# Performance work log

Hardware: AMD Instinct MI355X
Metric: run time of the kernel (lower is better)

## Reference

```python
import jax, jax.numpy as jnp
import numpy as np
import math

N_WAY, K_SHOT, Q_QUERY, PRJ_NUM, D = 5, 5, 15, 6, 64


def setup_inputs() -> dict:
    key = jax.random.key(0)
    k1, k2 = jax.random.split(key)
    feat = jax.random.normal(k1, (600, 64, 10, 10), dtype=jnp.float32)
    label = jax.random.randint(k2, (450,), 0, N_WAY)
    scale = jnp.ones((1,), dtype=jnp.float32)
    r = jnp.zeros((2,), dtype=jnp.float32)
    return {"feat": feat, "label": label, "scale": scale, "r": r}


def reference(feat, label, scale, r):
    ns = N_WAY * K_SHOT * PRJ_NUM  # 150 support images
    inv_sqrt_d = 1.0 / math.sqrt(D)
    support_xf = feat[:ns] * inv_sqrt_d
    query_xf = feat[ns:] * inv_sqrt_d
    q, c, h, w = query_xf.shape

    # support: (n_way, k_shot*prj_num*h*w, c)
    support = support_xf.reshape(N_WAY, K_SHOT * PRJ_NUM, c, h * w)
    support = jnp.transpose(support, (0, 1, 3, 2)).reshape(N_WAY, -1, c)
    # query: (q*h*w, c)
    query = jnp.transpose(query_xf.reshape(q, c, h * w), (0, 2, 1)).reshape(q * h * w, c)

    alpha, beta = r[0], r[1]
    reg = support.shape[1] / support.shape[2]
    lam = reg * jnp.exp(alpha)
    rho = jnp.exp(beta)

    # Woodbury / normal-equations path: hat = (S^T S + lam I)^-1 S^T S, per class
    sts = jnp.einsum('nkc,nkd->ncd', support, support)  # (n_way, c, c)
    m = sts + lam * jnp.eye(c, dtype=sts.dtype)[None]
    hat = jnp.linalg.inv(m) @ sts  # (n_way, c, c)

    Q_bar = jnp.einsum('qc,ncd->nqd', query, hat) * rho  # (n_way, q*h*w, c)
    dist = jnp.sum((Q_bar - query[None]) ** 2, axis=2).T  # (q*h*w, n_way)
    neg_l2_dist = -dist.reshape(q, h * w, N_WAY).mean(axis=1)  # (q, n_way)

    y_pred = jax.nn.softmax(neg_l2_dist, axis=1)
    logits = neg_l2_dist * scale[0]
    logp = jax.nn.log_softmax(logits, axis=1)
    loss = -jnp.mean(jnp.take_along_axis(logp, label[:, None], axis=1))
    return y_pred, loss
```

## Files before the change

kernel.cpp:

```cpp
#include <hip/hip_runtime.h>
#include <math.h>


typedef __attribute__((ext_vector_type(8))) short short8;
typedef __attribute__((ext_vector_type(4))) float f32x4;

#define NSUP 150
#define NQ 450
#define PIX 100
#define IMG_STRIDE 6400
#define MAGIC 0x5F3D2B1Cu

static __device__ __forceinline__ short bf16r(float x) {
  unsigned u = __builtin_bit_cast(unsigned, x);
  u += 0x7FFFu + ((u >> 16) & 1u);
  return (short)(u >> 16);
}
static __device__ __forceinline__ float b2f(short v) {
  return __builtin_bit_cast(float, ((unsigned)(unsigned short)v) << 16);
}
static __device__ __forceinline__ void st_flag(unsigned* p, unsigned v) {
  __threadfence();
  __hip_atomic_store(p, v, __ATOMIC_RELEASE, __HIP_MEMORY_SCOPE_AGENT);
}
static __device__ __forceinline__ void spin_flag(unsigned* p) {
  int guard = 1 << 22;
  while (__hip_atomic_load(p, __ATOMIC_ACQUIRE, __HIP_MEMORY_SCOPE_AGENT) != MAGIC
         && --guard) __builtin_amdgcn_s_sleep(2);
}

typedef const __attribute__((address_space(1))) void gas_void;
typedef __attribute__((address_space(3))) void las_void;
static __device__ __forceinline__ void gload1k(const float* src, float* dst, int lane) {
  __builtin_amdgcn_global_load_lds((gas_void*)(src + lane * 4), (las_void*)dst,
                                   16, 0, 0);
}

static __device__ __forceinline__ void gram_ks_lds(const float* img, f32x4 acc[4][4],
                                                   int ks, int r, int g) {
  short8 frag[4];
  const int kb = ks * 32 + g * 8;
  #pragma unroll
  for (int R = 0; R < 4; ++R) {
    short8 q;
    const float* p = img + (R * 16 + r) * PIX + kb;
    if (ks < 3) {
      float4 lo = *(const float4*)p;
      float4 hi = *(const float4*)(p + 4);
      q[0] = bf16r(lo.x); q[1] = bf16r(lo.y); q[2] = bf16r(lo.z); q[3] = bf16r(lo.w);
      q[4] = bf16r(hi.x); q[5] = bf16r(hi.y); q[6] = bf16r(hi.z); q[7] = bf16r(hi.w);
    } else if (g == 0) {
      float4 lo = *(const float4*)p;
      q[0] = bf16r(lo.x); q[1] = bf16r(lo.y); q[2] = bf16r(lo.z); q[3] = bf16r(lo.w);
      q[4] = 0; q[5] = 0; q[6] = 0; q[7] = 0;
    } else {
      #pragma unroll
      for (int j = 0; j < 8; ++j) q[j] = 0;
    }
    frag[R] = q;
  }
  #pragma unroll
  for (int R = 0; R < 4; ++R)
    #pragma unroll
    for (int C = 0; C < 4; ++C)
      acc[R][C] = __builtin_amdgcn_mfma_f32_16x16x32_bf16(frag[R], frag[C],
                                                          acc[R][C], 0, 0, 0);
}

static __device__ __forceinline__ void mm64q(const short* A, const short* B,
                                             f32x4 t[2][2], int r, int g,
                                             int wr, int wc) {
  #pragma unroll
  for (int ks = 0; ks < 2; ++ks) {
    short8 af[2], bfr[2];
    #pragma unroll
    for (int i = 0; i < 2; ++i) {
      af[i]  = *(const short8*)(A + (wr * 32 + i * 16 + r) * 72 + ks * 32 + g * 8);
      bfr[i] = *(const short8*)(B + (wc * 32 + i * 16 + r) * 72 + ks * 32 + g * 8);
    }
    #pragma unroll
    for (int i = 0; i < 2; ++i)
      #pragma unroll
      for (int j = 0; j < 2; ++j)
        t[i][j] = __builtin_amdgcn_mfma_f32_16x16x32_bf16(af[i], bfr[j],
                                                          t[i][j], 0, 0, 0);
  }
}

#define ZERO_ACC4(t)                                  \
  _Pragma("unroll") for (int R = 0; R < 4; ++R)       \
  _Pragma("unroll") for (int C = 0; C < 4; ++C)       \
  _Pragma("unroll") for (int q = 0; q < 4; ++q) t[R][C][q] = 0.f;

#define ZERO_ACC2(t)                                  \
  _Pragma("unroll") for (int R = 0; R < 2; ++R)       \
  _Pragma("unroll") for (int C = 0; C < 2; ++C)       \
  _Pragma("unroll") for (int q = 0; q < 4; ++q) t[R][C][q] = 0.f;

__global__ __launch_bounds__(256) void k_fused(
    const float* __restrict__ feat, const int* __restrict__ label,
    const float* __restrict__ scale, const float* __restrict__ rvec,
    float* __restrict__ out,
    float* __restrict__ partial,
    unsigned short* __restrict__ Gneg,
    float* __restrict__ blockloss,
    unsigned* __restrict__ gflag,
    unsigned* __restrict__ sflag,
    unsigned* __restrict__ lflag) {
  __shared__ __align__(16) char smem[65536];
  const int b = blockIdx.x, tid = threadIdx.x;
  const int wave = tid >> 6, lane = tid & 63;
  const int r = lane & 15, g = lane >> 4;

  if (b < 75) {
    float* img0 = (float*)smem;
    float* img1 = (float*)(smem + 25600);
    float (*gbuf)[4096] = (float (*)[4096])smem;
    const int cls = b / 15, grp = b % 15;
    const float* f0 = feat + (size_t)(cls * 30 + grp * 2) * IMG_STRIDE;
    const float* f1 = f0 + IMG_STRIDE;

    {
      const int beg = (wave < 2) ? wave * 13 : 26 + (wave - 2) * 12;
      const int cnt = (wave < 2) ? 13 : 12;
      for (int i = 0; i < cnt; ++i) {
        const int ch = beg + i;
        const float* src = (ch < 25) ? f0 + ch * 256 : f1 + (ch - 25) * 256;
        float* dst = (ch < 25) ? img0 + ch * 256 : img1 + (ch - 25) * 256;
        gload1k(src, dst, lane);
      }
    }
    asm volatile("s_waitcnt vmcnt(0)" ::: "memory");
    __syncthreads();

    f32x4 acc[4][4];
    ZERO_ACC4(acc)
    gram_ks_lds(img0, acc, wave, r, g);
    gram_ks_lds(img1, acc, wave, r, g);
    __syncthreads();

    #pragma unroll
    for (int R = 0; R < 4; ++R)
      #pragma unroll
      for (int C = 0; C < 4; ++C)
        #pragma unroll
        for (int q = 0; q < 4; ++q) {
          const int row = R * 16 + g * 4 + q, col = C * 16 + r;
          gbuf[wave][row * 64 + col] = acc[R][C][q];
        }
    __syncthreads();

    float* outp = partial + (size_t)b * 4096;
    for (int c = tid; c < 1024; c += 256) {
      f32x4 s0 = *(const f32x4*)&gbuf[0][4 * c];
      f32x4 s1 = *(const f32x4*)&gbuf[1][4 * c];
      f32x4 s2 = *(const f32x4*)&gbuf[2][4 * c];
      f32x4 s3 = *(const f32x4*)&gbuf[3][4 * c];
      f32x4 s = s0 + s1 + s2 + s3;
      *(float4*)(outp + 4 * c) = *(float4*)&s;
    }
    __syncthreads();
    if (tid == 0) st_flag(&gflag[b], MAGIC);
    return;
  }

  if (b < 80) {
    float* Ms   = (float*)(smem);
    short* Mb   = (short*)(smem + 16640);
    short* Tb   = (short*)(smem + 25856);
    short* Xa   = (short*)(smem + 35072);
    short* Xc   = (short*)(smem + 44288);
    float* radp = (float*)(smem + 53504);
    float* scal = (float*)(smem + 54528);

    const int n = b - 75;
    const int wr = wave >> 1, wc = wave & 1;
    const float lam = 46.875f * expf(rvec[0]);
    const float rho = expf(rvec[1]);

    if (tid < 15) spin_flag(&gflag[n * 15 + tid]);
    __syncthreads();

    {
      const float* base = partial + (size_t)n * 15 * 4096;
      for (int c = tid; c < 1024; c += 256) {
        float4 s = {0.f, 0.f, 0.f, 0.f};
        #pragma unroll
        for (int p = 0; p < 15; ++p) {
          float4 v = *(const float4*)(base + p * 4096 + 4 * c);
          s.x += v.x; s.y += v.y; s.z += v.z; s.w += v.w;
        }
        const int e = 4 * c, row = e >> 6, col = e & 63;
        Ms[row * 65 + col + 0] = s.x * (1.f / 64.f);
        Ms[row * 65 + col + 1] = s.y * (1.f / 64.f);
        Ms[row * 65 + col + 2] = s.z * (1.f / 64.f);
        Ms[row * 65 + col + 3] = s.w * (1.f / 64.f);
      }
    }
    __syncthreads();
    if (tid < 64) Ms[tid * 65 + tid] += lam;
    __syncthreads();

    {
      const int row = tid & 63, part = tid >> 6;
      float s = 0.f;
      #pragma unroll
      for (int k = 0; k < 16; ++k) s += fabsf(Ms[row * 65 + part * 16 + k]);
      radp[part * 64 + row] = s;
    }
    __syncthreads();
    if (tid < 64) {
      const float diag = Ms[tid * 65 + tid];
      const float rad = radp[tid] + radp[64 + tid] + radp[128 + tid] +
                        radp[192 + tid] - fabsf(diag);
      float lo = diag - rad, hi = diag + rad;
      for (int off = 32; off; off >>= 1) {
        lo = fminf(lo, __shfl_down(lo, off));
        hi = fmaxf(hi, __shfl_down(hi, off));
      }
      if (tid == 0) {
        const float a = fmaxf(lo, lam);
        const float bb = hi;
        const float s = a + bb, d = bb - a;
        scal[0] = s;
        scal[1] = 8.f / (2.f * s * s - d * d);
      }
    }
    __syncthreads();
    const float s0 = scal[0], theta = scal[1];

    for (int e = tid; e < 4096; e += 256) {
      const int i = e >> 6, j = e & 63;
      const float m = Ms[i * 65 + j];
      Mb[i * 72 + j] = bf16r(m);
      Xa[i * 72 + j] = bf16r(theta * (((i == j) ? s0 : 0.f) - m));
    }
    __syncthreads();

    short* x = Xa;
    short* xn = Xc;
    for (int it = 0; it < 2; ++it) {
      {
        f32x4 t[2][2];
        ZERO_ACC2(t)
        mm64q(x, Mb, t, r, g, wr, wc);
        #pragma unroll
        for (int i = 0; i < 2; ++i)
          #pragma unroll
          for (int j = 0; j < 2; ++j)
            #pragma unroll
            for (int q = 0; q < 4; ++q) {
              const int row = wr * 32 + i * 16 + g * 4 + q;
              const int col = wc * 32 + j * 16 + r;
              Tb[row * 72 + col] = bf16r(t[i][j][q]);
            }
      }
      __syncthreads();
      {
        f32x4 t[2][2];
        ZERO_ACC2(t)
        mm64q(Tb, x, t, r, g, wr, wc);
        #pragma unroll
        for (int i = 0; i < 2; ++i)
          #pragma unroll
          for (int j = 0; j < 2; ++j)
            #pragma unroll
            for (int q = 0; q < 4; ++q) {
              const int row = wr * 32 + i * 16 + g * 4 + q;
              const int col = wc * 32 + j * 16 + r;
              const int idx = row * 72 + col;
              xn[idx] = bf16r(2.f * b2f(x[idx]) - t[i][j][q]);
            }
      }
      __syncthreads();
      short* tmp = x; x = xn; xn = tmp;
    }

    for (int e = tid; e < 4096; e += 256) {
      const int i = e >> 6, j = e & 63;
      const float xv = b2f(x[i * 72 + j]);
      Tb[i * 72 + j] = bf16r(((i == j) ? (rho - 1.f) : 0.f) - rho * lam * xv);
    }
    __syncthreads();

    {
      f32x4 t[2][2];
      ZERO_ACC2(t)
      mm64q(Tb, Tb, t, r, g, wr, wc);
      #pragma unroll
      for (int i = 0; i < 2; ++i)
        #pragma unroll
        for (int j = 0; j < 2; ++j)
          #pragma unroll
          for (int q = 0; q < 4; ++q) {
            const int row = wr * 32 + i * 16 + g * 4 + q;
            const int col = wc * 32 + j * 16 + r;
            Gneg[n * 4096 + row * 64 + col] =
                (unsigned short)bf16r(t[i][j][q] * (-0.01f));
          }
    }
    __syncthreads();
    if (tid == 0) st_flag(&sflag[n], MAGIC);
    return;
  }

  const int qb = b - 80;
  float* imgA = (float*)smem;
  float* imgB = (float*)(smem + 25600);
  const int half = wave >> 1;
  const int gimg = qb * 2 + half;
  const float* fq = feat + (size_t)(NSUP + gimg) * IMG_STRIDE;
  float* mybuf = half ? imgB : imgA;

  {
    const int w2 = wave & 1;
    const int beg = w2 ? 13 : 0;
    const int cnt = w2 ? 12 : 13;
    for (int i = 0; i < cnt; ++i)
      gload1k(fq + (beg + i) * 256, mybuf + (beg + i) * 256, lane);
  }
  asm volatile("s_waitcnt vmcnt(0)" ::: "memory");
  __syncthreads();

  f32x4 acc[4][4];
  ZERO_ACC4(acc)
  const int kbase = (wave & 1) * 2;
  gram_ks_lds(mybuf, acc, kbase, r, g);
  gram_ks_lds(mybuf, acc, kbase + 1, r, g);
  __syncthreads();

  float* p1 = (float*)(smem + 32768);
  float* p3 = (float*)(smem + 49152);
  if (wave & 1) {
    float* dst = (wave == 1) ? p1 : p3;
    #pragma unroll
    for (int R = 0; R < 4; ++R)
      #pragma unroll
      for (int C = 0; C < 4; ++C)
        #pragma unroll
        for (int q = 0; q < 4; ++q) {
          const int row = R * 16 + g * 4 + q, col = C * 16 + r;
          dst[row * 64 + col] = acc[R][C][q];
        }
  }
  __syncthreads();
  if (!(wave & 1)) {
    const float* src = (wave == 0) ? p1 : p3;
    #pragma unroll
    for (int R = 0; R < 4; ++R)
      #pragma unroll
      for (int C = 0; C < 4; ++C)
        #pragma unroll
        for (int q = 0; q < 4; ++q) {
          const int row = R * 16 + g * 4 + q, col = C * 16 + r;
          acc[R][C][q] += src[row * 64 + col];
        }
  }

  if (tid < 5) spin_flag(&sflag[tid]);
  __syncthreads();

  unsigned short* Gs = (unsigned short*)smem;
  for (int e = tid; e < 2560; e += 256) {
    const int nn = e >> 9, rem = e & 511, row = rem >> 3, c8 = (rem & 7) << 3;
    *(short8*)&Gs[nn * 4608 + row * 72 + c8] =
        *(const short8*)&Gneg[nn * 4096 + row * 64 + c8];
  }
  __syncthreads();

  float* wl = (float*)(smem + 46080);
  if (!(wave & 1)) {
    float nl[5] = {0.f, 0.f, 0.f, 0.f, 0.f};
    #pragma unroll
    for (int R = 0; R < 4; ++R)
      #pragma unroll
      for (int C = 0; C < 4; ++C)
        #pragma unroll
        for (int q = 0; q < 4; ++q) {
          const int row = R * 16 + g * 4 + q, col = C * 16 + r;
          const float cv = acc[R][C][q] * (1.f / 64.f);
          const int idx = row * 72 + col;
          #pragma unroll
          for (int nn = 0; nn < 5; ++nn)
            nl[nn] += b2f((short)Gs[nn * 4608 + idx]) * cv;
        }
    #pragma unroll
    for (int nn = 0; nn < 5; ++nn)
      for (int off = 32; off; off >>= 1) nl[nn] += __shfl_down(nl[nn], off);

    if (lane == 0) {
      float mx = nl[0];
      #pragma unroll
      for (int nn = 1; nn < 5; ++nn) mx = fmaxf(mx, nl[nn]);
      float ex[5], se = 0.f;
      #pragma unroll
      for (int nn = 0; nn < 5; ++nn) { ex[nn] = expf(nl[nn] - mx); se += ex[nn]; }
      const float inv = 1.f / se;
      #pragma unroll
      for (int nn = 0; nn < 5; ++nn) out[gimg * 5 + nn] = ex[nn] * inv;

      const float sc = scale[0];
      float mx2 = nl[0] * sc;
      #pragma unroll
      for (int nn = 1; nn < 5; ++nn) mx2 = fmaxf(mx2, nl[nn] * sc);
      float se2 = 0.f;
      #pragma unroll
      for (int nn = 0; nn < 5; ++nn) se2 += expf(nl[nn] * sc - mx2);
      wl[half] = mx2 + logf(se2) - nl[label[gimg]] * sc;
    }
  }
  __syncthreads();
  if (tid == 0) {
    blockloss[qb] = wl[0] + wl[1];
    st_flag(&lflag[qb], MAGIC);
  }

  if (qb == 0 && wave == 0) {
    for (int i = lane; i < 225; i += 64) spin_flag(&lflag[i]);
    float s = 0.f;
    for (int i = lane; i < 225; i += 64) s += blockloss[i];
    for (int off = 32; off; off >>= 1) s += __shfl_down(s, off);
    if (lane == 0) out[2250] = s / 450.f;
  }
}

extern "C" void kernel_launch(void* const* d_in, const int* in_sizes, int n_in,
                              void* d_out, int out_size, void* d_ws, size_t ws_size,
                              hipStream_t stream) {
  const float* feat  = (const float*)d_in[0];
  const int*   label = (const int*)d_in[1];
  const float* scale = (const float*)d_in[2];
  const float* rvec  = (const float*)d_in[3];
  float* out = (float*)d_out;

  char* ws = (char*)d_ws;
  float*          partial   = (float*)ws;
  unsigned short* Gneg      = (unsigned short*)(ws + 1228800);
  float*          blockloss = (float*)(ws + 1269760);
  unsigned*       flags     = (unsigned*)(ws + 1270784);
  unsigned* gflag = flags;
  unsigned* sflag = flags + 80;
  unsigned* lflag = flags + 96;

  k_fused<<<dim3(305), dim3(256), 0, stream>>>(feat, label, scale, rvec, out,
                                               partial, Gneg, blockloss,
                                               gflag, sflag, lflag);
}
```

Measured before the change: 28.33 us.

## Load features directly from global, interleave class G matrices, relax flag atomics

Measured after the change: 27.19 us. -4.0%, faster.

```diff
diff --git a/kernel.cpp b/kernel.cpp
--- a/kernel.cpp
+++ b/kernel.cpp
@@ -20,30 +20,23 @@
   return __builtin_bit_cast(float, ((unsigned)(unsigned short)v) << 16);
 }
 static __device__ __forceinline__ void st_flag(unsigned* p, unsigned v) {
-  __threadfence();
-  __hip_atomic_store(p, v, __ATOMIC_RELEASE, __HIP_MEMORY_SCOPE_AGENT);
-}
-static __device__ __forceinline__ void spin_flag(unsigned* p) {
+  __builtin_amdgcn_fence(__ATOMIC_RELEASE, "agent");
+  __hip_atomic_store(p, v, __ATOMIC_RELAXED, __HIP_MEMORY_SCOPE_AGENT);
+}
+static __device__ __forceinline__ void spin_rlx(unsigned* p) {
   int guard = 1 << 22;
-  while (__hip_atomic_load(p, __ATOMIC_ACQUIRE, __HIP_MEMORY_SCOPE_AGENT) != MAGIC
+  while (__hip_atomic_load(p, __ATOMIC_RELAXED, __HIP_MEMORY_SCOPE_AGENT) != MAGIC
          && --guard) __builtin_amdgcn_s_sleep(2);
 }
 
-typedef const __attribute__((address_space(1))) void gas_void;
-typedef __attribute__((address_space(3))) void las_void;
-static __device__ __forceinline__ void gload1k(const float* src, float* dst, int lane) {
-  __builtin_amdgcn_global_load_lds((gas_void*)(src + lane * 4), (las_void*)dst,
-                                   16, 0, 0);
-}
-
-static __device__ __forceinline__ void gram_ks_lds(const float* img, f32x4 acc[4][4],
-                                                   int ks, int r, int g) {
+static __device__ __forceinline__ void gram_ks(const float* __restrict__ f,
+                                               f32x4 acc[4][4], int ks, int r, int g) {
   short8 frag[4];
   const int kb = ks * 32 + g * 8;
   #pragma unroll
   for (int R = 0; R < 4; ++R) {
     short8 q;
-    const float* p = img + (R * 16 + r) * PIX + kb;
+    const float* p = f + (R * 16 + r) * PIX + kb;
     if (ks < 3) {
       float4 lo = *(const float4*)p;
       float4 hi = *(const float4*)(p + 4);
@@ -102,61 +95,57 @@
     const float* __restrict__ scale, const float* __restrict__ rvec,
     float* __restrict__ out,
     float* __restrict__ partial,
-    unsigned short* __restrict__ Gneg,
+    unsigned short* __restrict__ G01h,
+    unsigned short* __restrict__ G23h,
+    unsigned short* __restrict__ G4h,
     float* __restrict__ blockloss,
     unsigned* __restrict__ gflag,
     unsigned* __restrict__ sflag,
     unsigned* __restrict__ lflag) {
-  __shared__ __align__(16) char smem[65536];
+  __shared__ __align__(16) char smem[55296];
   const int b = blockIdx.x, tid = threadIdx.x;
   const int wave = tid >> 6, lane = tid & 63;
   const int r = lane & 15, g = lane >> 4;
 
   if (b < 75) {
-    float* img0 = (float*)smem;
-    float* img1 = (float*)(smem + 25600);
-    float (*gbuf)[4096] = (float (*)[4096])smem;
+    float (*sbuf)[4096] = (float (*)[4096])smem;
     const int cls = b / 15, grp = b % 15;
     const float* f0 = feat + (size_t)(cls * 30 + grp * 2) * IMG_STRIDE;
-    const float* f1 = f0 + IMG_STRIDE;
-
-    {
-      const int beg = (wave < 2) ? wave * 13 : 26 + (wave - 2) * 12;
-      const int cnt = (wave < 2) ? 13 : 12;
-      for (int i = 0; i < cnt; ++i) {
-        const int ch = beg + i;
-        const float* src = (ch < 25) ? f0 + ch * 256 : f1 + (ch - 25) * 256;
-        float* dst = (ch < 25) ? img0 + ch * 256 : img1 + (ch - 25) * 256;
-        gload1k(src, dst, lane);
-      }
-    }
-    asm volatile("s_waitcnt vmcnt(0)" ::: "memory");
-    __syncthreads();
-
     f32x4 acc[4][4];
     ZERO_ACC4(acc)
-    gram_ks_lds(img0, acc, wave, r, g);
-    gram_ks_lds(img1, acc, wave, r, g);
-    __syncthreads();
-
-    #pragma unroll
-    for (int R = 0; R < 4; ++R)
-      #pragma unroll
-      for (int C = 0; C < 4; ++C)
-        #pragma unroll
-        for (int q = 0; q < 4; ++q) {
-          const int row = R * 16 + g * 4 + q, col = C * 16 + r;
-          gbuf[wave][row * 64 + col] = acc[R][C][q];
-        }
-    __syncthreads();
-
+    gram_ks(f0, acc, wave, r, g);
+    gram_ks(f0 + IMG_STRIDE, acc, wave, r, g);
+
+    if (wave) {
+      #pragma unroll
+      for (int R = 0; R < 4; ++R)
+        #pragma unroll
+        for (int C = 0; C < 4; ++C)
+          #pragma unroll
+          for (int q = 0; q < 4; ++q) {
+            const int row = R * 16 + g * 4 + q, col = C * 16 + r;
+            sbuf[wave - 1][row * 64 + col] = acc[R][C][q];
+          }
+    }
+    __syncthreads();
+    if (!wave) {
+      #pragma unroll
+      for (int R = 0; R < 4; ++R)
+        #pragma unroll
+        for (int C = 0; C < 4; ++C)
+          #pragma unroll
+          for (int q = 0; q < 4; ++q) {
+            const int row = R * 16 + g * 4 + q, col = C * 16 + r;
+            sbuf[0][row * 64 + col] += acc[R][C][q];
+          }
+    }
+    __syncthreads();
     float* outp = partial + (size_t)b * 4096;
     for (int c = tid; c < 1024; c += 256) {
-      f32x4 s0 = *(const f32x4*)&gbuf[0][4 * c];
-      f32x4 s1 = *(const f32x4*)&gbuf[1][4 * c];
-      f32x4 s2 = *(const f32x4*)&gbuf[2][4 * c];
-      f32x4 s3 = *(const f32x4*)&gbuf[3][4 * c];
-      f32x4 s = s0 + s1 + s2 + s3;
+      f32x4 s0 = *(const f32x4*)&sbuf[0][4 * c];
+      f32x4 s1 = *(const f32x4*)&sbuf[1][4 * c];
+      f32x4 s2 = *(const f32x4*)&sbuf[2][4 * c];
+      f32x4 s = s0 + s1 + s2;
       *(float4*)(outp + 4 * c) = *(float4*)&s;
     }
     __syncthreads();
@@ -178,8 +167,9 @@
     const float lam = 46.875f * expf(rvec[0]);
     const float rho = expf(rvec[1]);
 
-    if (tid < 15) spin_flag(&gflag[n * 15 + tid]);
-    __syncthreads();
+    if (tid < 15) spin_rlx(&gflag[n * 15 + tid]);
+    __syncthreads();
+    __builtin_amdgcn_fence(__ATOMIC_ACQUIRE, "agent");
 
     {
       const float* base = partial + (size_t)n * 15 * 4096;
@@ -287,6 +277,9 @@
       f32x4 t[2][2];
       ZERO_ACC2(t)
       mm64q(Tb, Tb, t, r, g, wr, wc);
+      unsigned short* baseh = (n < 2) ? G01h : (n < 4) ? G23h : G4h;
+      const int off = (n < 4) ? (n & 1) : 0;
+      const int mul = (n < 4) ? 2 : 1;
       #pragma unroll
       for (int i = 0; i < 2; ++i)
         #pragma unroll
@@ -295,7 +288,7 @@
           for (int q = 0; q < 4; ++q) {
             const int row = wr * 32 + i * 16 + g * 4 + q;
             const int col = wc * 32 + j * 16 + r;
-            Gneg[n * 4096 + row * 64 + col] =
+            baseh[(row * 64 + col) * mul + off] =
                 (unsigned short)bf16r(t[i][j][q] * (-0.01f));
           }
     }
@@ -305,118 +298,112 @@
   }
 
   const int qb = b - 80;
-  float* imgA = (float*)smem;
-  float* imgB = (float*)(smem + 25600);
   const int half = wave >> 1;
   const int gimg = qb * 2 + half;
   const float* fq = feat + (size_t)(NSUP + gimg) * IMG_STRIDE;
-  float* mybuf = half ? imgB : imgA;
-
-  {
-    const int w2 = wave & 1;
-    const int beg = w2 ? 13 : 0;
-    const int cnt = w2 ? 12 : 13;
-    for (int i = 0; i < cnt; ++i)
-      gload1k(fq + (beg + i) * 256, mybuf + (beg + i) * 256, lane);
-  }
-  asm volatile("s_waitcnt vmcnt(0)" ::: "memory");
-  __syncthreads();
-
   f32x4 acc[4][4];
   ZERO_ACC4(acc)
-  const int kbase = (wave & 1) * 2;
-  gram_ks_lds(mybuf, acc, kbase, r, g);
-  gram_ks_lds(mybuf, acc, kbase + 1, r, g);
+  const int ksb = (wave & 1) * 2;
+  gram_ks(fq, acc, ksb, r, g);
+  gram_ks(fq, acc, ksb + 1, r, g);
+
+  if (tid == 0) {
+    int guard = 1 << 20;
+    for (;;) {
+      unsigned x = 0;
+      #pragma unroll
+      for (int i = 0; i < 5; ++i)
+        x |= __hip_atomic_load(&sflag[i], __ATOMIC_RELAXED,
+                               __HIP_MEMORY_SCOPE_AGENT) ^ MAGIC;
+      if (x == 0 || --guard == 0) break;
+      __builtin_amdgcn_s_sleep(4);
+    }
+  }
   __syncthreads();
-
-  float* p1 = (float*)(smem + 32768);
-  float* p3 = (float*)(smem + 49152);
-  if (wave & 1) {
-    float* dst = (wave == 1) ? p1 : p3;
-    #pragma unroll
-    for (int R = 0; R < 4; ++R)
-      #pragma unroll
-      for (int C = 0; C < 4; ++C)
-        #pragma unroll
-        for (int q = 0; q < 4; ++q) {
-          const int row = R * 16 + g * 4 + q, col = C * 16 + r;
-          dst[row * 64 + col] = acc[R][C][q];
-        }
+  __builtin_amdgcn_fence(__ATOMIC_ACQUIRE, "agent");
+
+  unsigned*       G01s = (unsigned*)smem;
+  unsigned*       G23s = (unsigned*)(smem + 17408);
+  unsigned short* G4s  = (unsigned short*)(smem + 34816);
+  {
+    const unsigned* G01w = (const unsigned*)G01h;
+    const unsigned* G23w = (const unsigned*)G23h;
+    for (int e = tid; e < 4096; e += 256) {
+      const int row = e >> 6, col = e & 63;
+      G01s[row * 68 + col] = G01w[e];
+      G23s[row * 68 + col] = G23w[e];
+    }
+    const unsigned* G4w = (const unsigned*)G4h;
+    unsigned* G4sw = (unsigned*)G4s;
+    for (int e = tid; e < 2048; e += 256) {
+      const int row = e >> 5, cw = e & 31;
+      G4sw[row * 34 + cw] = G4w[e];
+    }
   }
   __syncthreads();
-  if (!(wave & 1)) {
-    const float* src = (wave == 0) ? p1 : p3;
-    #pragma unroll
-    for (int R = 0; R < 4; ++R)
-      #pragma unroll
-      for (int C = 0; C < 4; ++C)
-        #pragma unroll
-        for (int q = 0; q < 4; ++q) {
-          const int row = R * 16 + g * 4 + q, col = C * 16 + r;
-          acc[R][C][q] += src[row * 64 + col];
-        }
-  }
-
-  if (tid < 5) spin_flag(&sflag[tid]);
+
+  float nl[5] = {0.f, 0.f, 0.f, 0.f, 0.f};
+  #pragma unroll
+  for (int R = 0; R < 4; ++R)
+    #pragma unroll
+    for (int C = 0; C < 4; ++C)
+      #pragma unroll
+      for (int q = 0; q < 4; ++q) {
+        const int row = R * 16 + g * 4 + q, col = C * 16 + r;
+        const float cv = acc[R][C][q] * (1.f / 64.f);
+        const int i68 = row * 68 + col;
+        const unsigned v01 = G01s[i68], v23 = G23s[i68];
+        nl[0] += b2f((short)(v01 & 0xffff)) * cv;
+        nl[1] += b2f((short)(v01 >> 16)) * cv;
+        nl[2] += b2f((short)(v23 & 0xffff)) * cv;
+        nl[3] += b2f((short)(v23 >> 16)) * cv;
+        nl[4] += b2f((short)G4s[i68]) * cv;
+      }
+  #pragma unroll
+  for (int nn = 0; nn < 5; ++nn)
+    for (int off = 32; off; off >>= 1) nl[nn] += __shfl_down(nl[nn], off);
+
+  float* wl  = (float*)(smem + 43520);
+  float* wl2 = (float*)(smem + 43600);
+  if (lane == 0) {
+    #pragma unroll
+    for (int nn = 0; nn < 5; ++nn) wl[wave * 5 + nn] = nl[nn];
+  }
   __syncthreads();
-
-  unsigned short* Gs = (unsigned short*)smem;
-  for (int e = tid; e < 2560; e += 256) {
-    const int nn = e >> 9, rem = e & 511, row = rem >> 3, c8 = (rem & 7) << 3;
-    *(short8*)&Gs[nn * 4608 + row * 72 + c8] =
-        *(const short8*)&Gneg[nn * 4096 + row * 64 + c8];
-  }
-  __syncthreads();
-
-  float* wl = (float*)(smem + 46080);
-  if (!(wave & 1)) {
-    float nl[5] = {0.f, 0.f, 0.f, 0.f, 0.f};
-    #pragma unroll
-    for (int R = 0; R < 4; ++R)
-      #pragma unroll
-      for (int C = 0; C < 4; ++C)
-        #pragma unroll
-        for (int q = 0; q < 4; ++q) {
-          const int row = R * 16 + g * 4 + q, col = C * 16 + r;
-          const float cv = acc[R][C][q] * (1.f / 64.f);
-          const int idx = row * 72 + col;
-          #pragma unroll
-          for (int nn = 0; nn < 5; ++nn)
-            nl[nn] += b2f((short)Gs[nn * 4608 + idx]) * cv;
-        }
+  if ((wave & 1) == 0 && lane == 0) {
+    float nlf[5];
     #pragma unroll
     for (int nn = 0; nn < 5; ++nn)
-      for (int off = 32; off; off >>= 1) nl[nn] += __shfl_down(nl[nn], off);
-
-    if (lane == 0) {
-      float mx = nl[0];
-      #pragma unroll
-      for (int nn = 1; nn < 5; ++nn) mx = fmaxf(mx, nl[nn]);
-      float ex[5], se = 0.f;
-      #pragma unroll
-      for (int nn = 0; nn < 5; ++nn) { ex[nn] = expf(nl[nn] - mx); se += ex[nn]; }
-      const float inv = 1.f / se;
-      #pragma unroll
-      for (int nn = 0; nn < 5; ++nn) out[gimg * 5 + nn] = ex[nn] * inv;
-
-      const float sc = scale[0];
-      float mx2 = nl[0] * sc;
-      #pragma unroll
-      for (int nn = 1; nn < 5; ++nn) mx2 = fmaxf(mx2, nl[nn] * sc);
-      float se2 = 0.f;
-      #pragma unroll
-      for (int nn = 0; nn < 5; ++nn) se2 += expf(nl[nn] * sc - mx2);
-      wl[half] = mx2 + logf(se2) - nl[label[gimg]] * sc;
-    }
+      nlf[nn] = wl[wave * 5 + nn] + wl[(wave + 1) * 5 + nn];
+
+    float mx = nlf[0];
+    #pragma unroll
+    for (int nn = 1; nn < 5; ++nn) mx = fmaxf(mx, nlf[nn]);
+    float ex[5], se = 0.f;
+    #pragma unroll
+    for (int nn = 0; nn < 5; ++nn) { ex[nn] = expf(nlf[nn] - mx); se += ex[nn]; }
+    const float inv = 1.f / se;
+    #pragma unroll
+    for (int nn = 0; nn < 5; ++nn) out[gimg * 5 + nn] = ex[nn] * inv;
+
+    const float sc = scale[0];
+    float mx2 = nlf[0] * sc;
+    #pragma unroll
+    for (int nn = 1; nn < 5; ++nn) mx2 = fmaxf(mx2, nlf[nn] * sc);
+    float se2 = 0.f;
+    #pragma unroll
+    for (int nn = 0; nn < 5; ++nn) se2 += expf(nlf[nn] * sc - mx2);
+    wl2[half] = mx2 + logf(se2) - nlf[label[gimg]] * sc;
   }
   __syncthreads();
   if (tid == 0) {
-    blockloss[qb] = wl[0] + wl[1];
+    blockloss[qb] = wl2[0] + wl2[1];
     st_flag(&lflag[qb], MAGIC);
   }
 
   if (qb == 0 && wave == 0) {
-    for (int i = lane; i < 225; i += 64) spin_flag(&lflag[i]);
+    for (int i = lane; i < 225; i += 64) spin_rlx(&lflag[i]);
+    __builtin_amdgcn_fence(__ATOMIC_ACQUIRE, "agent");
     float s = 0.f;
     for (int i = lane; i < 225; i += 64) s += blockloss[i];
     for (int off = 32; off; off >>= 1) s += __shfl_down(s, off);
@@ -435,7 +422,9 @@
 
   char* ws = (char*)d_ws;
   float*          partial   = (float*)ws;
-  unsigned short* Gneg      = (unsigned short*)(ws + 1228800);
+  unsigned short* G01h      = (unsigned short*)(ws + 1228800);
+  unsigned short* G23h      = (unsigned short*)(ws + 1245184);
+  unsigned short* G4h       = (unsigned short*)(ws + 1261568);
   float*          blockloss = (float*)(ws + 1269760);
   unsigned*       flags     = (unsigned*)(ws + 1270784);
   unsigned* gflag = flags;
@@ -443,6 +432,6 @@
   unsigned* lflag = flags + 96;
 
   k_fused<<<dim3(305), dim3(256), 0, stream>>>(feat, label, scale, rvec, out,
-                                               partial, Gneg, blockloss,
-                                               gflag, sflag, lflag);
-}
+                                               partial, G01h, G23h, G4h,
+                                               blockloss, gflag, sflag, lflag);
+}
```
